# Kernel tuning notes

Hardware: AMD Instinct MI355X
Metric: run time of the kernel (lower is better)

Reference implementation:

```python
import jax, jax.numpy as jnp
import numpy as np

N = 16384; E = 262144; G = 32; NPG = N // G
D_FEAT = 256; AA_DIM = 64; N_LABELS = 21
H0, O0 = 2, 64      # layer0: in 320 -> 2 heads x 64, flatten -> 128
H1, O1 = 2, 256     # out layer: in 128 -> 2 heads x 256, mean over heads -> 256
NCLS = 2
NEG_SLOPE = 0.2     # DGL GATConv LeakyReLU default


def setup_inputs() -> dict:
    key = jax.random.key(0)
    ks = jax.random.split(key, 32)

    def gn(k, shape, fan):
        return jax.random.normal(k, shape, dtype=jnp.float32) / np.float32(np.sqrt(fan))

    din0 = AA_DIM + D_FEAT
    din1 = H0 * O0
    inp = {}
    inp['feat'] = jax.random.normal(ks[0], (N, D_FEAT), dtype=jnp.float32)
    inp['aa_emb'] = gn(ks[1], (N_LABELS, AA_DIM), 1.0)
    inp['W0'] = gn(ks[2], (din0, H0 * O0), din0)
    inp['al0'] = gn(ks[3], (H0, O0), O0)
    inp['ar0'] = gn(ks[4], (H0, O0), O0)
    inp['res0'] = gn(ks[5], (din0, H0 * O0), din0)
    inp['b0'] = jnp.zeros((H0 * O0,), jnp.float32)
    inp['W1'] = gn(ks[6], (din1, H1 * O1), din1)
    inp['al1'] = gn(ks[7], (H1, O1), O1)
    inp['ar1'] = gn(ks[8], (H1, O1), O1)
    inp['res1'] = gn(ks[9], (din1, H1 * O1), din1)
    inp['b1'] = jnp.zeros((H1 * O1,), jnp.float32)
    inp['mW0'] = gn(ks[10], (O1, O1 // 2), O1)
    inp['mb0'] = jnp.zeros((O1 // 2,), jnp.float32)
    inp['mW1'] = gn(ks[11], (O1 // 2, O1 // 4), O1 // 2)
    inp['mb1'] = jnp.zeros((O1 // 4,), jnp.float32)
    inp['mW2'] = gn(ks[12], (O1 // 4, NCLS), O1 // 4)
    inp['mb2'] = jnp.zeros((NCLS,), jnp.float32)
    inp['ref_aa'] = jax.random.randint(ks[13], (N,), 0, N_LABELS)
    inp['alt_aa'] = jax.random.randint(ks[14], (G,), 0, N_LABELS)
    inp['src'] = jax.random.randint(ks[15], (E,), 0, N)
    inp['dst'] = jax.random.randint(ks[16], (E,), 0, N)
    inp['graph_id'] = jnp.arange(N) // NPG   # 512 nodes per graph, contiguous
    return inp


def _gat_conv(h, src, dst, W, al, ar, resW, bias, heads, out, act):
    n = h.shape[0]
    ft = (h @ W).reshape(n, heads, out)                # [N,H,O] projected src/dst feats
    el = jnp.einsum('nho,ho->nh', ft, al)
    er = jnp.einsum('nho,ho->nh', ft, ar)
    e = el[src] + er[dst]                              # [E,H]
    e = jnp.where(e > 0, e, NEG_SLOPE * e)             # LeakyReLU
    # edge softmax over incoming edges of each dst node
    emax = jax.ops.segment_max(e, dst, num_segments=n)
    ez = jnp.exp(e - emax[dst])
    denom = jax.ops.segment_sum(ez, dst, num_segments=n)
    alpha = ez / denom[dst]                            # [E,H]
    rst = jax.ops.segment_sum(ft[src] * alpha[:, :, None], dst, num_segments=n)
    rst = rst + (h @ resW).reshape(n, heads, out) + bias.reshape(1, heads, out)
    return act(rst) if act is not None else rst


def _forward(feat, aa_emb, W0, al0, ar0, res0, b0, W1, al1, ar1, res1, b1,
             mW0, mb0, mW1, mb1, mW2, mb2, ref_aa, alt_aa, src, dst, graph_id):
    # per-node ref amino-acid embedding gated by per-graph alt embedding
    h_aa = aa_emb[ref_aa] * aa_emb[alt_aa][graph_id]   # [N, AA_DIM]
    h = jnp.concatenate([h_aa, feat], axis=-1)         # [N, 320]
    h = _gat_conv(h, src, dst, W0, al0, ar0, res0, b0, H0, O0, jax.nn.elu).reshape(N, -1)
    h = _gat_conv(h, src, dst, W1, al1, ar1, res1, b1, H1, O1, None)   # [N,H1,O1]
    h = jax.nn.elu(jnp.mean(h, axis=1))                # mean over heads -> [N, O1]
    hg = jax.ops.segment_sum(h, graph_id, num_segments=G) / np.float32(NPG)  # mean readout
    x = jnp.maximum(hg @ mW0 + mb0, 0.0)               # MLPReadout (L=2, ReLU)
    x = jnp.maximum(x @ mW1 + mb1, 0.0)
    return x @ mW2 + mb2                               # [G, NCLS] logits


def reference(feat, aa_emb, W0, al0, ar0, res0, b0, W1, al1, ar1, res1, b1,
              mW0, mb0, mW1, mb1, mW2, mb2, ref_aa, alt_aa, src, dst, graph_id):
    return _forward(feat, aa_emb, W0, al0, ar0, res0, b0, W1, al1, ar1, res1, b1,
                    mW0, mb0, mW1, mb1, mW2, mb2, ref_aa, alt_aa, src, dst, graph_id)
```

## Files before the change

### kernel.cpp

```cpp
#include <hip/hip_runtime.h>
#include <hip/hip_bf16.h>

#define NN 16384
#define EE 262144
#define GG 32
#define NPGC 512
#define NEG_SLOPE 0.2f

typedef __attribute__((ext_vector_type(8))) short bf16x8;
typedef __attribute__((ext_vector_type(4))) float f32x4;

__device__ __forceinline__ float b2f(short s) {
    union { float f; unsigned u; } c;
    c.u = ((unsigned)(unsigned short)s) << 16;
    return c.f;
}

__device__ __forceinline__ short f2b(float f) {
    __hip_bfloat16 b = __float2bfloat16(f);
    short r;
    __builtin_memcpy(&r, &b, 2);
    return r;
}

__global__ __launch_bounds__(320) void build_h_kernel(
    const float* __restrict__ feat, const float* __restrict__ aa_emb,
    const int* __restrict__ ref_aa, const int* __restrict__ alt_aa,
    const int* __restrict__ graph_id, __hip_bfloat16* __restrict__ h,
    int* __restrict__ deg)
{
    int n = blockIdx.x, t = threadIdx.x;
    if (t == 0) deg[n] = 0;
    float v;
    if (t < 64) {
        int ra = ref_aa[n], ga = alt_aa[graph_id[n]];
        v = aa_emb[ra * 64 + t] * aa_emb[ga * 64 + t];
    } else {
        v = feat[(size_t)n * 256 + (t - 64)];
    }
    h[(size_t)n * 320 + t] = __float2bfloat16(v);
}

__global__ __launch_bounds__(256) void wtrans_kernel(
    const float* __restrict__ W0, const float* __restrict__ R0,
    const float* __restrict__ W1, const float* __restrict__ R1,
    __hip_bfloat16* __restrict__ wt0, __hip_bfloat16* __restrict__ wt1)
{
    int k = blockIdx.x * 256 + threadIdx.x;
    int c = blockIdx.y;
    if (c < 256) {
        if (k >= 320) return;
        float v = (c < 128) ? W0[(size_t)k * 128 + c] : R0[(size_t)k * 128 + (c - 128)];
        wt0[(size_t)c * 320 + k] = __float2bfloat16(v);
    } else {
        int cc = c - 256;
        if (k >= 128) return;
        float v = (cc < 512) ? W1[(size_t)k * 512 + cc] : R1[(size_t)k * 512 + (cc - 512)];
        wt1[(size_t)cc * 128 + k] = __float2bfloat16(v);
    }
}

__global__ __launch_bounds__(256) void deg_kernel(const int* __restrict__ dst, int* __restrict__ deg)
{
    int i = blockIdx.x * 256 + threadIdx.x;
    if (i < EE) atomicAdd(&deg[dst[i]], 1);
}

__global__ __launch_bounds__(256) void scan_kernel(const int* __restrict__ deg,
                                                   int* __restrict__ row, int* __restrict__ cursor)
{
    __shared__ int part[256];
    __shared__ int pref[257];
    int t = threadIdx.x, base = t * 64;
    int s = 0;
    for (int i = 0; i < 64; i++) s += deg[base + i];
    part[t] = s;
    __syncthreads();
    if (t == 0) {
        int a = 0;
        for (int i = 0; i < 256; i++) { pref[i] = a; a += part[i]; }
        pref[256] = a;
    }
    __syncthreads();
    int a = pref[t];
    for (int i = 0; i < 64; i++) {
        row[base + i] = a; cursor[base + i] = a;
        a += deg[base + i];
    }
    if (t == 0) row[NN] = pref[256];
}

__global__ __launch_bounds__(256) void scatter_kernel(
    const int* __restrict__ src, const int* __restrict__ dst,
    int* __restrict__ cursor, int* __restrict__ srcs)
{
    int i = blockIdx.x * 256 + threadIdx.x;
    if (i < EE) {
        int p = atomicAdd(&cursor[dst[i]], 1);
        srcs[p] = src[i];
    }
}

template<int FR, int C1, int KTOT>
__global__ __launch_bounds__(256) void mfma_gemm_kernel(
    const __hip_bfloat16* __restrict__ A, const __hip_bfloat16* __restrict__ Bt,
    __hip_bfloat16* __restrict__ ftb, float* __restrict__ resf)
{
    constexpr int BM = 32 * FR;
    __shared__ short As[BM * 64];
    __shared__ short Bs[BM * 64];
    int t = threadIdx.x;
    int wid = t >> 6, lane = t & 63;
    int wr = wid >> 1, wc = wid & 1;
    int row0 = blockIdx.x * BM, col0 = blockIdx.y * BM;

    f32x4 acc[FR][FR];
#pragma unroll
    for (int m = 0; m < FR; m++)
#pragma unroll
        for (int n = 0; n < FR; n++) acc[m][n] = (f32x4){0.f, 0.f, 0.f, 0.f};

    for (int kk = 0; kk < KTOT; kk += 64) {
        __syncthreads();
#pragma unroll
        for (int c = t; c < BM * 8; c += 256) {
            int row = c >> 3, slot = c & 7;
            int sw = (slot ^ (row & 7)) * 8;
            bf16x8 va = *(const bf16x8*)(A + (size_t)(row0 + row) * KTOT + kk + slot * 8);
            *(bf16x8*)(&As[row * 64 + sw]) = va;
            bf16x8 vb = *(const bf16x8*)(Bt + (size_t)(col0 + row) * KTOT + kk + slot * 8);
            *(bf16x8*)(&Bs[row * 64 + sw]) = vb;
        }
        __syncthreads();
#pragma unroll
        for (int ks = 0; ks < 2; ks++) {
            int kslot = ks * 4 + (lane >> 4);
            bf16x8 a[FR], b[FR];
#pragma unroll
            for (int m = 0; m < FR; m++) {
                int row = wr * FR * 16 + m * 16 + (lane & 15);
                a[m] = *(const bf16x8*)(&As[row * 64 + ((kslot ^ (row & 7)) * 8)]);
            }
#pragma unroll
            for (int n = 0; n < FR; n++) {
                int col = wc * FR * 16 + n * 16 + (lane & 15);
                b[n] = *(const bf16x8*)(&Bs[col * 64 + ((kslot ^ (col & 7)) * 8)]);
            }
#pragma unroll
            for (int m = 0; m < FR; m++)
#pragma unroll
                for (int n = 0; n < FR; n++)
                    acc[m][n] = __builtin_amdgcn_mfma_f32_16x16x32_bf16(a[m], b[n], acc[m][n], 0, 0, 0);
        }
    }

#pragma unroll
    for (int m = 0; m < FR; m++)
#pragma unroll
        for (int n = 0; n < FR; n++) {
            int colg = col0 + wc * FR * 16 + n * 16 + (lane & 15);
            int rbase = row0 + wr * FR * 16 + m * 16 + (lane >> 4) * 4;
#pragma unroll
            for (int r = 0; r < 4; r++) {
                float v = acc[m][n][r];
                int rg = rbase + r;
                if (colg < C1) ftb[(size_t)rg * C1 + colg] = __float2bfloat16(v);
                else           resf[(size_t)rg * C1 + (colg - C1)] = v;
            }
        }
}

__global__ __launch_bounds__(256) void elr0_kernel(
    const __hip_bfloat16* __restrict__ ftb,
    const float* __restrict__ al, const float* __restrict__ ar,
    float* __restrict__ el, float* __restrict__ er)
{
    int gid = blockIdx.x * 256 + threadIdx.x;
    int wv = gid >> 6, lane = gid & 63;
    int n = wv >> 1, hh = wv & 1;
    if (n >= NN) return;
    float f = b2f(((const short*)ftb)[(size_t)n * 128 + hh * 64 + lane]);
    float sl = f * al[hh * 64 + lane];
    float sr = f * ar[hh * 64 + lane];
#pragma unroll
    for (int d = 32; d; d >>= 1) { sl += __shfl_xor(sl, d); sr += __shfl_xor(sr, d); }
    if (lane == 0) { el[n * 2 + hh] = sl; er[n * 2 + hh] = sr; }
}

__global__ __launch_bounds__(256) void elr1_kernel(
    const __hip_bfloat16* __restrict__ ftb,
    const float* __restrict__ al, const float* __restrict__ ar,
    float* __restrict__ el, float* __restrict__ er)
{
    int wv = (blockIdx.x * 256 + threadIdx.x) >> 6;
    int lane = threadIdx.x & 63;
    if (wv >= NN) return;
    int n = wv, hh = lane >> 5, dim = lane * 8;
    bf16x8 v = *(const bf16x8*)((const short*)ftb + (size_t)n * 512 + dim);
    float sl = 0.f, sr = 0.f;
#pragma unroll
    for (int j = 0; j < 8; j++) {
        float f = b2f(v[j]);
        sl += f * al[dim + j];
        sr += f * ar[dim + j];
    }
#pragma unroll
    for (int d = 16; d; d >>= 1) { sl += __shfl_xor(sl, d); sr += __shfl_xor(sr, d); }
    if ((lane & 31) == 0) { el[n * 2 + hh] = sl; er[n * 2 + hh] = sr; }
}

__global__ __launch_bounds__(256) void agg0_kernel(
    const __hip_bfloat16* __restrict__ ftb0, const float* __restrict__ resf0,
    const int* __restrict__ row, const int* __restrict__ srcs,
    const float* __restrict__ el, const float* __restrict__ er,
    const float* __restrict__ b0, __hip_bfloat16* __restrict__ h1)
{
    int wv = (blockIdx.x * 256 + threadIdx.x) >> 6;
    int lane = threadIdx.x & 63;
    if (wv >= NN) return;
    int n = wv;
    int eo = lane >> 4, vo = lane & 15;
    int hh = vo >> 3, dim = vo * 8;
    int e0 = row[n], e1 = row[n + 1];
    float er0v = er[n * 2 + 0], er1v = er[n * 2 + 1];

    float acc[8] = {0.f, 0.f, 0.f, 0.f, 0.f, 0.f, 0.f, 0.f};
    float ts0 = 0.f, ts1 = 0.f;
    for (int base = e0; base < e1; base += 64) {
        int c = min(64, e1 - base);
        float w0 = 0.f, w1 = 0.f;
        int sm = -1;
        if (lane < c) {
            sm = srcs[base + lane];
            float v0 = el[sm * 2 + 0] + er0v; v0 = v0 > 0.f ? v0 : NEG_SLOPE * v0;
            float v1 = el[sm * 2 + 1] + er1v; v1 = v1 > 0.f ? v1 : NEG_SLOPE * v1;
            w0 = __expf(v0); w1 = __expf(v1);
        }
        ts0 += w0; ts1 += w1;
        for (int i = eo; i < c; i += 4) {
            int s = __shfl(sm, i);
            float a0 = __shfl(w0, i), a1 = __shfl(w1, i);
            float a = hh ? a1 : a0;
            bf16x8 v = *(const bf16x8*)((const short*)ftb0 + (size_t)s * 128 + dim);
#pragma unroll
            for (int j = 0; j < 8; j++) acc[j] += a * b2f(v[j]);
        }
    }
#pragma unroll
    for (int d = 32; d; d >>= 1) { ts0 += __shfl_xor(ts0, d); ts1 += __shfl_xor(ts1, d); }
#pragma unroll
    for (int j = 0; j < 8; j++) acc[j] += __shfl_xor(acc[j], 16);
#pragma unroll
    for (int j = 0; j < 8; j++) acc[j] += __shfl_xor(acc[j], 32);
    if (eo == 0) {
        float s = hh ? ts1 : ts0;
        float invv = s > 0.f ? 1.f / s : 0.f;
        const float* resp = resf0 + (size_t)n * 128 + dim;
        bf16x8 o;
#pragma unroll
        for (int j = 0; j < 8; j++) {
            float r = acc[j] * invv + resp[j] + b0[dim + j];
            r = r > 0.f ? r : (__expf(r) - 1.f);
            o[j] = f2b(r);
        }
        *(bf16x8*)((short*)h1 + (size_t)n * 128 + dim) = o;
    }
}

__global__ __launch_bounds__(256) void agg1_kernel(
    const __hip_bfloat16* __restrict__ ftb1, const float* __restrict__ resf1,
    const int* __restrict__ row, const int* __restrict__ srcs,
    const float* __restrict__ el, const float* __restrict__ er,
    const float* __restrict__ b1, float* __restrict__ h2)
{
    int wv = (blockIdx.x * 256 + threadIdx.x) >> 6;
    int lane = threadIdx.x & 63;
    if (wv >= NN) return;
    int n = wv;
    int hh = lane >> 5, dim = lane * 8;
    int e0 = row[n], e1 = row[n + 1];
    float er0v = er[n * 2 + 0], er1v = er[n * 2 + 1];

    float acc[8] = {0.f, 0.f, 0.f, 0.f, 0.f, 0.f, 0.f, 0.f};
    float ts0 = 0.f, ts1 = 0.f;
    for (int base = e0; base < e1; base += 64) {
        int c = min(64, e1 - base);
        float w0 = 0.f, w1 = 0.f;
        int sm = -1;
        if (lane < c) {
            sm = srcs[base + lane];
            float v0 = el[sm * 2 + 0] + er0v; v0 = v0 > 0.f ? v0 : NEG_SLOPE * v0;
            float v1 = el[sm * 2 + 1] + er1v; v1 = v1 > 0.f ? v1 : NEG_SLOPE * v1;
            w0 = __expf(v0); w1 = __expf(v1);
        }
        ts0 += w0; ts1 += w1;
        int i = 0;
        for (; i + 4 <= c; i += 4) {
            int sA = __shfl(sm, i),     sB = __shfl(sm, i + 1);
            int sC = __shfl(sm, i + 2), sD = __shfl(sm, i + 3);
            float a0A = __shfl(w0, i),     a1A = __shfl(w1, i);
            float a0B = __shfl(w0, i + 1), a1B = __shfl(w1, i + 1);
            float a0C = __shfl(w0, i + 2), a1C = __shfl(w1, i + 2);
            float a0D = __shfl(w0, i + 3), a1D = __shfl(w1, i + 3);
            float aA = hh ? a1A : a0A, aB = hh ? a1B : a0B;
            float aC = hh ? a1C : a0C, aD = hh ? a1D : a0D;
            bf16x8 vA = *(const bf16x8*)((const short*)ftb1 + (size_t)sA * 512 + dim);
            bf16x8 vB = *(const bf16x8*)((const short*)ftb1 + (size_t)sB * 512 + dim);
            bf16x8 vC = *(const bf16x8*)((const short*)ftb1 + (size_t)sC * 512 + dim);
            bf16x8 vD = *(const bf16x8*)((const short*)ftb1 + (size_t)sD * 512 + dim);
#pragma unroll
            for (int j = 0; j < 8; j++) {
                acc[j] += aA * b2f(vA[j]) + aB * b2f(vB[j]) + aC * b2f(vC[j]) + aD * b2f(vD[j]);
            }
        }
        for (; i < c; i++) {
            int s = __shfl(sm, i);
            float a0 = __shfl(w0, i), a1 = __shfl(w1, i);
            float a = hh ? a1 : a0;
            bf16x8 v = *(const bf16x8*)((const short*)ftb1 + (size_t)s * 512 + dim);
#pragma unroll
            for (int j = 0; j < 8; j++) acc[j] += a * b2f(v[j]);
        }
    }
#pragma unroll
    for (int d = 32; d; d >>= 1) { ts0 += __shfl_xor(ts0, d); ts1 += __shfl_xor(ts1, d); }
    float s = hh ? ts1 : ts0;
    float invv = s > 0.f ? 1.f / s : 0.f;

    const float* resp = resf1 + (size_t)n * 512 + dim;
    float r[8];
#pragma unroll
    for (int j = 0; j < 8; j++)
        r[j] = acc[j] * invv + resp[j] + b1[dim + j];
    float v[8];
#pragma unroll
    for (int j = 0; j < 8; j++) {
        float o = __shfl_xor(r[j], 32);
        v[j] = 0.5f * (r[j] + o);
    }
    if (lane < 32) {
#pragma unroll
        for (int j = 0; j < 8; j++) {
            float x = v[j];
            v[j] = x > 0.f ? x : (__expf(x) - 1.f);
        }
        float* outp = h2 + (size_t)n * 256 + lane * 8;
        *(f32x4*)outp = (f32x4){v[0], v[1], v[2], v[3]};
        *(f32x4*)(outp + 4) = (f32x4){v[4], v[5], v[6], v[7]};
    }
}

__global__ __launch_bounds__(256) void readout1_kernel(
    const float* __restrict__ h2, float* __restrict__ part)
{
    int blk = blockIdx.x;
    int g = blk >> 4, c = blk & 15;
    int t = threadIdx.x;
    float s = 0.f;
    int base = g * NPGC + c * 32;
    for (int i = 0; i < 32; i++) s += h2[(size_t)(base + i) * 256 + t];
    part[(size_t)blk * 256 + t] = s;
}

__global__ __launch_bounds__(256) void readout2_kernel(
    const float* __restrict__ part,
    const float* __restrict__ mW0, const float* __restrict__ mb0,
    const float* __restrict__ mW1, const float* __restrict__ mb1,
    const float* __restrict__ mW2, const float* __restrict__ mb2,
    float* __restrict__ out)
{
    __shared__ float hg[256];
    __shared__ float x1[128];
    __shared__ float x2[64];
    int g = blockIdx.x, t = threadIdx.x;
    float s = 0.f;
    for (int c = 0; c < 16; c++) s += part[(size_t)(g * 16 + c) * 256 + t];
    hg[t] = s * (1.f / (float)NPGC);
    __syncthreads();
    if (t < 128) {
        float a = mb0[t];
        for (int k = 0; k < 256; k++) a += hg[k] * mW0[k * 128 + t];
        x1[t] = fmaxf(a, 0.f);
    }
    __syncthreads();
    if (t < 64) {
        float a = mb1[t];
        for (int k = 0; k < 128; k++) a += x1[k] * mW1[k * 64 + t];
        x2[t] = fmaxf(a, 0.f);
    }
    __syncthreads();
    if (t < 2) {
        float a = mb2[t];
        for (int k = 0; k < 64; k++) a += x2[k] * mW2[k * 2 + t];
        out[g * 2 + t] = a;
    }
}

extern "C" void kernel_launch(void* const* d_in, const int* in_sizes, int n_in,
                              void* d_out, int out_size, void* d_ws, size_t ws_size,
                              hipStream_t stream)
{
    const float* feat   = (const float*)d_in[0];
    const float* aa_emb = (const float*)d_in[1];
    const float* W0     = (const float*)d_in[2];
    const float* al0    = (const float*)d_in[3];
    const float* ar0    = (const float*)d_in[4];
    const float* res0   = (const float*)d_in[5];
    const float* b0     = (const float*)d_in[6];
    const float* W1     = (const float*)d_in[7];
    const float* al1    = (const float*)d_in[8];
    const float* ar1    = (const float*)d_in[9];
    const float* res1   = (const float*)d_in[10];
    const float* b1     = (const float*)d_in[11];
    const float* mW0    = (const float*)d_in[12];
    const float* mb0    = (const float*)d_in[13];
    const float* mW1    = (const float*)d_in[14];
    const float* mb1    = (const float*)d_in[15];
    const float* mW2    = (const float*)d_in[16];
    const float* mb2    = (const float*)d_in[17];
    const int* ref_aa   = (const int*)d_in[18];
    const int* alt_aa   = (const int*)d_in[19];
    const int* src      = (const int*)d_in[20];
    const int* dst      = (const int*)d_in[21];
    const int* graph_id = (const int*)d_in[22];
    float* out = (float*)d_out;

    size_t off = 0;
    auto alloc = [&](size_t bytes) -> void* {
        void* p = (char*)d_ws + off;
        off += (bytes + 255) & ~(size_t)255;
        return p;
    };
    __hip_bfloat16* h    = (__hip_bfloat16*)alloc((size_t)NN * 320 * 2);
    __hip_bfloat16* wt0  = (__hip_bfloat16*)alloc((size_t)256 * 320 * 2);
    __hip_bfloat16* wt1  = (__hip_bfloat16*)alloc((size_t)1024 * 128 * 2);
    __hip_bfloat16* ftb0 = (__hip_bfloat16*)alloc((size_t)NN * 128 * 2);
    float* resf0  = (float*)alloc((size_t)NN * 128 * 4);
    __hip_bfloat16* h1b  = (__hip_bfloat16*)alloc((size_t)NN * 128 * 2);
    __hip_bfloat16* ftb1 = (__hip_bfloat16*)alloc((size_t)NN * 512 * 2);
    float* resf1  = (float*)alloc((size_t)NN * 512 * 4);
    float* h2     = (float*)alloc((size_t)NN * 256 * 4);
    float* el0    = (float*)alloc((size_t)NN * 2 * 4);
    float* er0    = (float*)alloc((size_t)NN * 2 * 4);
    float* el1    = (float*)alloc((size_t)NN * 2 * 4);
    float* er1    = (float*)alloc((size_t)NN * 2 * 4);
    int* deg      = (int*)alloc((size_t)NN * 4);
    int* row      = (int*)alloc((size_t)(NN + 1) * 4);
    int* cursor   = (int*)alloc((size_t)NN * 4);
    int* srcs     = (int*)alloc((size_t)EE * 4);
    float* part   = (float*)alloc((size_t)GG * 16 * 256 * 4);

    (void)in_sizes; (void)n_in; (void)out_size; (void)ws_size;

    build_h_kernel<<<NN, 320, 0, stream>>>(feat, aa_emb, ref_aa, alt_aa, graph_id, h, deg);
    wtrans_kernel<<<dim3(2, 1280), 256, 0, stream>>>(W0, res0, W1, res1, wt0, wt1);
    deg_kernel<<<EE / 256, 256, 0, stream>>>(dst, deg);
    scan_kernel<<<1, 256, 0, stream>>>(deg, row, cursor);
    scatter_kernel<<<EE / 256, 256, 0, stream>>>(src, dst, cursor, srcs);

    mfma_gemm_kernel<2, 128, 320><<<dim3(256, 4), 256, 0, stream>>>(h, wt0, ftb0, resf0);
    elr0_kernel<<<(NN * 2 * 64) / 256, 256, 0, stream>>>(ftb0, al0, ar0, el0, er0);
    agg0_kernel<<<NN / 4, 256, 0, stream>>>(ftb0, resf0, row, srcs, el0, er0, b0, h1b);

    mfma_gemm_kernel<4, 512, 128><<<dim3(128, 8), 256, 0, stream>>>(h1b, wt1, ftb1, resf1);
    elr1_kernel<<<NN / 4, 256, 0, stream>>>(ftb1, al1, ar1, el1, er1);
    agg1_kernel<<<NN / 4, 256, 0, stream>>>(ftb1, resf1, row, srcs, el1, er1, b1, h2);

    readout1_kernel<<<GG * 16, 256, 0, stream>>>(h2, part);
    readout2_kernel<<<GG, 256, 0, stream>>>(part, mW0, mb0, mW1, mb1, mW2, mb2, out);
}
```

Baseline: 165.5 us.

## Merge independent kernels and fuse readout partial sums into layer-1 aggregation

```diff
diff --git a/kernel.cpp b/kernel.cpp
--- a/kernel.cpp
+++ b/kernel.cpp
@@ -23,96 +23,53 @@
     return r;
 }
 
-__global__ __launch_bounds__(320) void build_h_kernel(
+__global__ __launch_bounds__(320) void prep_kernel(
     const float* __restrict__ feat, const float* __restrict__ aa_emb,
     const int* __restrict__ ref_aa, const int* __restrict__ alt_aa,
     const int* __restrict__ graph_id, __hip_bfloat16* __restrict__ h,
-    int* __restrict__ deg)
-{
-    int n = blockIdx.x, t = threadIdx.x;
-    if (t == 0) deg[n] = 0;
-    float v;
-    if (t < 64) {
-        int ra = ref_aa[n], ga = alt_aa[graph_id[n]];
-        v = aa_emb[ra * 64 + t] * aa_emb[ga * 64 + t];
-    } else {
-        v = feat[(size_t)n * 256 + (t - 64)];
-    }
-    h[(size_t)n * 320 + t] = __float2bfloat16(v);
-}
-
-__global__ __launch_bounds__(256) void wtrans_kernel(
+    int* __restrict__ deg,
     const float* __restrict__ W0, const float* __restrict__ R0,
     const float* __restrict__ W1, const float* __restrict__ R1,
     __hip_bfloat16* __restrict__ wt0, __hip_bfloat16* __restrict__ wt1)
 {
-    int k = blockIdx.x * 256 + threadIdx.x;
-    int c = blockIdx.y;
-    if (c < 256) {
-        if (k >= 320) return;
-        float v = (c < 128) ? W0[(size_t)k * 128 + c] : R0[(size_t)k * 128 + (c - 128)];
-        wt0[(size_t)c * 320 + k] = __float2bfloat16(v);
+    int b = blockIdx.x, t = threadIdx.x;
+    if (b < NN) {
+        int n = b;
+        if (t == 0) deg[n] = 0;
+        float v;
+        if (t < 64) {
+            int ra = ref_aa[n], ga = alt_aa[graph_id[n]];
+            v = aa_emb[ra * 64 + t] * aa_emb[ga * 64 + t];
+        } else {
+            v = feat[(size_t)n * 256 + (t - 64)];
+        }
+        h[(size_t)n * 320 + t] = __float2bfloat16(v);
+    } else if (b < NN + 256) {
+        int c = b - NN;
+        float v = (c < 128) ? W0[(size_t)t * 128 + c] : R0[(size_t)t * 128 + (c - 128)];
+        wt0[(size_t)c * 320 + t] = __float2bfloat16(v);
     } else {
-        int cc = c - 256;
-        if (k >= 128) return;
-        float v = (cc < 512) ? W1[(size_t)k * 512 + cc] : R1[(size_t)k * 512 + (cc - 512)];
-        wt1[(size_t)cc * 128 + k] = __float2bfloat16(v);
-    }
-}
-
-__global__ __launch_bounds__(256) void deg_kernel(const int* __restrict__ dst, int* __restrict__ deg)
-{
-    int i = blockIdx.x * 256 + threadIdx.x;
-    if (i < EE) atomicAdd(&deg[dst[i]], 1);
-}
-
-__global__ __launch_bounds__(256) void scan_kernel(const int* __restrict__ deg,
-                                                   int* __restrict__ row, int* __restrict__ cursor)
-{
-    __shared__ int part[256];
-    __shared__ int pref[257];
-    int t = threadIdx.x, base = t * 64;
-    int s = 0;
-    for (int i = 0; i < 64; i++) s += deg[base + i];
-    part[t] = s;
-    __syncthreads();
-    if (t == 0) {
-        int a = 0;
-        for (int i = 0; i < 256; i++) { pref[i] = a; a += part[i]; }
-        pref[256] = a;
-    }
-    __syncthreads();
-    int a = pref[t];
-    for (int i = 0; i < 64; i++) {
-        row[base + i] = a; cursor[base + i] = a;
-        a += deg[base + i];
-    }
-    if (t == 0) row[NN] = pref[256];
-}
-
-__global__ __launch_bounds__(256) void scatter_kernel(
-    const int* __restrict__ src, const int* __restrict__ dst,
-    int* __restrict__ cursor, int* __restrict__ srcs)
-{
-    int i = blockIdx.x * 256 + threadIdx.x;
-    if (i < EE) {
-        int p = atomicAdd(&cursor[dst[i]], 1);
-        srcs[p] = src[i];
+        int cc = b - NN - 256;
+        if (t < 128) {
+            float v = (cc < 512) ? W1[(size_t)t * 512 + cc] : R1[(size_t)t * 512 + (cc - 512)];
+            wt1[(size_t)cc * 128 + t] = __float2bfloat16(v);
+        }
     }
 }
 
 template<int FR, int C1, int KTOT>
-__global__ __launch_bounds__(256) void mfma_gemm_kernel(
+__device__ __forceinline__ void gemm_body(
     const __hip_bfloat16* __restrict__ A, const __hip_bfloat16* __restrict__ Bt,
-    __hip_bfloat16* __restrict__ ftb, float* __restrict__ resf)
+    __hip_bfloat16* __restrict__ ftb, float* __restrict__ resf,
+    int bx, int by, short* lds)
 {
     constexpr int BM = 32 * FR;
-    __shared__ short As[BM * 64];
-    __shared__ short Bs[BM * 64];
+    short* As = lds;
+    short* Bs = lds + BM * 64;
     int t = threadIdx.x;
     int wid = t >> 6, lane = t & 63;
     int wr = wid >> 1, wc = wid & 1;
-    int row0 = blockIdx.x * BM, col0 = blockIdx.y * BM;
+    int row0 = bx * BM, col0 = by * BM;
 
     f32x4 acc[FR][FR];
 #pragma unroll
@@ -135,7 +92,7 @@
 #pragma unroll
         for (int ks = 0; ks < 2; ks++) {
             int kslot = ks * 4 + (lane >> 4);
-            bf16x8 a[FR], b[FR];
+            bf16x8 a[FR], bfr[FR];
 #pragma unroll
             for (int m = 0; m < FR; m++) {
                 int row = wr * FR * 16 + m * 16 + (lane & 15);
@@ -144,13 +101,13 @@
 #pragma unroll
             for (int n = 0; n < FR; n++) {
                 int col = wc * FR * 16 + n * 16 + (lane & 15);
-                b[n] = *(const bf16x8*)(&Bs[col * 64 + ((kslot ^ (col & 7)) * 8)]);
+                bfr[n] = *(const bf16x8*)(&Bs[col * 64 + ((kslot ^ (col & 7)) * 8)]);
             }
 #pragma unroll
             for (int m = 0; m < FR; m++)
 #pragma unroll
                 for (int n = 0; n < FR; n++)
-                    acc[m][n] = __builtin_amdgcn_mfma_f32_16x16x32_bf16(a[m], b[n], acc[m][n], 0, 0, 0);
+                    acc[m][n] = __builtin_amdgcn_mfma_f32_16x16x32_bf16(a[m], bfr[n], acc[m][n], 0, 0, 0);
         }
     }
 
@@ -170,21 +127,79 @@
         }
 }
 
-__global__ __launch_bounds__(256) void elr0_kernel(
+__global__ __launch_bounds__(256) void gemm0_deg_kernel(
+    const __hip_bfloat16* __restrict__ A, const __hip_bfloat16* __restrict__ Bt,
+    __hip_bfloat16* __restrict__ ftb, float* __restrict__ resf,
+    const int* __restrict__ dst, int* __restrict__ deg)
+{
+    __shared__ short lds[2 * 64 * 64];
+    int b = blockIdx.x;
+    if (b < 1024) {
+        gemm_body<2, 128, 320>(A, Bt, ftb, resf, b & 255, b >> 8, lds);
+    } else {
+        int i = (b - 1024) * 256 + threadIdx.x;
+        if (i < EE) atomicAdd(&deg[dst[i]], 1);
+    }
+}
+
+__global__ __launch_bounds__(256) void gemm1_kernel(
+    const __hip_bfloat16* __restrict__ A, const __hip_bfloat16* __restrict__ Bt,
+    __hip_bfloat16* __restrict__ ftb, float* __restrict__ resf)
+{
+    __shared__ short lds[2 * 128 * 64];
+    gemm_body<4, 512, 128>(A, Bt, ftb, resf, blockIdx.x, blockIdx.y, lds);
+}
+
+__global__ __launch_bounds__(256) void scan_elr0_kernel(
+    const int* __restrict__ deg, int* __restrict__ row, int* __restrict__ cursor,
     const __hip_bfloat16* __restrict__ ftb,
     const float* __restrict__ al, const float* __restrict__ ar,
     float* __restrict__ el, float* __restrict__ er)
 {
-    int gid = blockIdx.x * 256 + threadIdx.x;
-    int wv = gid >> 6, lane = gid & 63;
-    int n = wv >> 1, hh = wv & 1;
-    if (n >= NN) return;
-    float f = b2f(((const short*)ftb)[(size_t)n * 128 + hh * 64 + lane]);
-    float sl = f * al[hh * 64 + lane];
-    float sr = f * ar[hh * 64 + lane];
-#pragma unroll
-    for (int d = 32; d; d >>= 1) { sl += __shfl_xor(sl, d); sr += __shfl_xor(sr, d); }
-    if (lane == 0) { el[n * 2 + hh] = sl; er[n * 2 + hh] = sr; }
+    int b = blockIdx.x, t = threadIdx.x;
+    if (b == 0) {
+        __shared__ int part[256];
+        __shared__ int pref[257];
+        int base = t * 64;
+        int s = 0;
+        for (int i = 0; i < 64; i++) s += deg[base + i];
+        part[t] = s;
+        __syncthreads();
+        if (t == 0) {
+            int a = 0;
+            for (int i = 0; i < 256; i++) { pref[i] = a; a += part[i]; }
+            pref[256] = a;
+        }
+        __syncthreads();
+        int a = pref[t];
+        for (int i = 0; i < 64; i++) {
+            row[base + i] = a; cursor[base + i] = a;
+            a += deg[base + i];
+        }
+        if (t == 0) row[NN] = pref[256];
+    } else {
+        int gid = (b - 1) * 256 + t;
+        int wv = gid >> 6, lane = gid & 63;
+        int n = wv >> 1, hh = wv & 1;
+        if (n >= NN) return;
+        float f = b2f(((const short*)ftb)[(size_t)n * 128 + hh * 64 + lane]);
+        float sl = f * al[hh * 64 + lane];
+        float sr = f * ar[hh * 64 + lane];
+#pragma unroll
+        for (int d = 32; d; d >>= 1) { sl += __shfl_xor(sl, d); sr += __shfl_xor(sr, d); }
+        if (lane == 0) { el[n * 2 + hh] = sl; er[n * 2 + hh] = sr; }
+    }
+}
+
+__global__ __launch_bounds__(256) void scatter_kernel(
+    const int* __restrict__ src, const int* __restrict__ dst,
+    int* __restrict__ cursor, int* __restrict__ srcs)
+{
+    int i = blockIdx.x * 256 + threadIdx.x;
+    if (i < EE) {
+        int p = atomicAdd(&cursor[dst[i]], 1);
+        srcs[p] = src[i];
+    }
 }
 
 __global__ __launch_bounds__(256) void elr1_kernel(
@@ -271,12 +286,12 @@
     const __hip_bfloat16* __restrict__ ftb1, const float* __restrict__ resf1,
     const int* __restrict__ row, const int* __restrict__ srcs,
     const float* __restrict__ el, const float* __restrict__ er,
-    const float* __restrict__ b1, float* __restrict__ h2)
-{
-    int wv = (blockIdx.x * 256 + threadIdx.x) >> 6;
-    int lane = threadIdx.x & 63;
-    if (wv >= NN) return;
-    int n = wv;
+    const float* __restrict__ b1, float* __restrict__ part)
+{
+    __shared__ float red[4][256];
+    int t = threadIdx.x;
+    int lane = t & 63, wid = t >> 6;
+    int n = blockIdx.x * 4 + wid;
     int hh = lane >> 5, dim = lane * 8;
     int e0 = row[n], e1 = row[n + 1];
     float er0v = er[n * 2 + 0], er1v = er[n * 2 + 1];
@@ -342,24 +357,12 @@
 #pragma unroll
         for (int j = 0; j < 8; j++) {
             float x = v[j];
-            v[j] = x > 0.f ? x : (__expf(x) - 1.f);
-        }
-        float* outp = h2 + (size_t)n * 256 + lane * 8;
-        *(f32x4*)outp = (f32x4){v[0], v[1], v[2], v[3]};
-        *(f32x4*)(outp + 4) = (f32x4){v[4], v[5], v[6], v[7]};
-    }
-}
-
-__global__ __launch_bounds__(256) void readout1_kernel(
-    const float* __restrict__ h2, float* __restrict__ part)
-{
-    int blk = blockIdx.x;
-    int g = blk >> 4, c = blk & 15;
-    int t = threadIdx.x;
-    float s = 0.f;
-    int base = g * NPGC + c * 32;
-    for (int i = 0; i < 32; i++) s += h2[(size_t)(base + i) * 256 + t];
-    part[(size_t)blk * 256 + t] = s;
+            x = x > 0.f ? x : (__expf(x) - 1.f);
+            red[wid][lane * 8 + j] = x;
+        }
+    }
+    __syncthreads();
+    part[(size_t)blockIdx.x * 256 + t] = red[0][t] + red[1][t] + red[2][t] + red[3][t];
 }
 
 __global__ __launch_bounds__(256) void readout2_kernel(
@@ -374,7 +377,7 @@
     __shared__ float x2[64];
     int g = blockIdx.x, t = threadIdx.x;
     float s = 0.f;
-    for (int c = 0; c < 16; c++) s += part[(size_t)(g * 16 + c) * 256 + t];
+    for (int c = 0; c < 128; c++) s += part[(size_t)(g * 128 + c) * 256 + t];
     hg[t] = s * (1.f / (float)NPGC);
     __syncthreads();
     if (t < 128) {
@@ -439,7 +442,6 @@
     __hip_bfloat16* h1b  = (__hip_bfloat16*)alloc((size_t)NN * 128 * 2);
     __hip_bfloat16* ftb1 = (__hip_bfloat16*)alloc((size_t)NN * 512 * 2);
     float* resf1  = (float*)alloc((size_t)NN * 512 * 4);
-    float* h2     = (float*)alloc((size_t)NN * 256 * 4);
     float* el0    = (float*)alloc((size_t)NN * 2 * 4);
     float* er0    = (float*)alloc((size_t)NN * 2 * 4);
     float* el1    = (float*)alloc((size_t)NN * 2 * 4);
@@ -448,24 +450,18 @@
     int* row      = (int*)alloc((size_t)(NN + 1) * 4);
     int* cursor   = (int*)alloc((size_t)NN * 4);
     int* srcs     = (int*)alloc((size_t)EE * 4);
-    float* part   = (float*)alloc((size_t)GG * 16 * 256 * 4);
+    float* part   = (float*)alloc((size_t)(NN / 4) * 256 * 4);
 
     (void)in_sizes; (void)n_in; (void)out_size; (void)ws_size;
 
-    build_h_kernel<<<NN, 320, 0, stream>>>(feat, aa_emb, ref_aa, alt_aa, graph_id, h, deg);
-    wtrans_kernel<<<dim3(2, 1280), 256, 0, stream>>>(W0, res0, W1, res1, wt0, wt1);
-    deg_kernel<<<EE / 256, 256, 0, stream>>>(dst, deg);
-    scan_kernel<<<1, 256, 0, stream>>>(deg, row, cursor);
+    prep_kernel<<<NN + 256 + 1024, 320, 0, stream>>>(
+        feat, aa_emb, ref_aa, alt_aa, graph_id, h, deg, W0, res0, W1, res1, wt0, wt1);
+    gemm0_deg_kernel<<<2048, 256, 0, stream>>>(h, wt0, ftb0, resf0, dst, deg);
+    scan_elr0_kernel<<<1 + 8192, 256, 0, stream>>>(deg, row, cursor, ftb0, al0, ar0, el0, er0);
     scatter_kernel<<<EE / 256, 256, 0, stream>>>(src, dst, cursor, srcs);
-
-    mfma_gemm_kernel<2, 128, 320><<<dim3(256, 4), 256, 0, stream>>>(h, wt0, ftb0, resf0);
-    elr0_kernel<<<(NN * 2 * 64) / 256, 256, 0, stream>>>(ftb0, al0, ar0, el0, er0);
     agg0_kernel<<<NN / 4, 256, 0, stream>>>(ftb0, resf0, row, srcs, el0, er0, b0, h1b);
-
-    mfma_gemm_kernel<4, 512, 128><<<dim3(128, 8), 256, 0, stream>>>(h1b, wt1, ftb1, resf1);
+    gemm1_kernel<<<dim3(128, 8), 256, 0, stream>>>(h1b, wt1, ftb1, resf1);
     elr1_kernel<<<NN / 4, 256, 0, stream>>>(ftb1, al1, ar1, el1, er1);
-    agg1_kernel<<<NN / 4, 256, 0, stream>>>(ftb1, resf1, row, srcs, el1, er1, b1, h2);
-
-    readout1_kernel<<<GG * 16, 256, 0, stream>>>(h2, part);
+    agg1_kernel<<<NN / 4, 256, 0, stream>>>(ftb1, resf1, row, srcs, el1, er1, b1, part);
     readout2_kernel<<<GG, 256, 0, stream>>>(part, mW0, mb0, mW1, mb1, mW2, mb2, out);
 }
```

Result: faster. 153.3 us (-7.4%).
